# Kernel optimization log

Measured on AMD Instinct MI355X. Metric: run time of the kernel, lower is better.

The kernel has to match this reference:

```python
import jax, jax.numpy as jnp
from jax import lax
import numpy as np

GRID = 8
H384 = 6 * GRID * GRID  # 384, LSTM input and hidden size


def _conv(x, w, b):
    # x: [B,C,H,W], w: [O,I,kh,kw]
    y = lax.conv_general_dilated(x, w, (1, 1), 'VALID',
                                 dimension_numbers=('NCHW', 'OIHW', 'NCHW'))
    return y + b[None, :, None, None]


def _maxpool2(x):
    return lax.reduce_window(x, -jnp.inf, lax.max,
                             (1, 1, 2, 2), (1, 1, 2, 2), 'VALID')


def setup_inputs() -> dict:
    key = jax.random.key(0)
    ks = jax.random.split(key, 20)
    s = 0.05
    d = {
        'x': jax.random.normal(ks[0], (512, 100, 100), jnp.float32),
        # conv stack: Conv2d(1,16,7) ... Conv2d(128,128,3)
        'cw1': jax.random.normal(ks[1], (16, 1, 7, 7), jnp.float32) * s,
        'cb1': jnp.zeros((16,), jnp.float32),
        'cw2': jax.random.normal(ks[2], (32, 16, 4, 4), jnp.float32) * s,
        'cb2': jnp.zeros((32,), jnp.float32),
        'cw3': jax.random.normal(ks[3], (64, 32, 5, 5), jnp.float32) * s,
        'cb3': jnp.zeros((64,), jnp.float32),
        'cw4': jax.random.normal(ks[4], (128, 64, 5, 5), jnp.float32) * s,
        'cb4': jnp.zeros((128,), jnp.float32),
        'cw5': jax.random.normal(ks[5], (128, 128, 5, 5), jnp.float32) * s,
        'cb5': jnp.zeros((128,), jnp.float32),
        'cw6': jax.random.normal(ks[6], (128, 128, 3, 3), jnp.float32) * s,
        'cb6': jnp.zeros((128,), jnp.float32),
        # linear layers: 8192 -> 1024 -> 384, Sigmoid
        'lw1': jax.random.normal(ks[7], (1024, 8192), jnp.float32) * 0.01,
        'lb1': jnp.zeros((1024,), jnp.float32),
        'lw2': jax.random.normal(ks[8], (384, 1024), jnp.float32) * 0.02,
        'lb2': jnp.zeros((384,), jnp.float32),
        # LSTM (input 384, hidden 384, 1 layer), torch gate order i,f,g,o
        'w_ih': jax.random.normal(ks[9], (4 * H384, H384), jnp.float32) * s,
        'w_hh': jax.random.normal(ks[10], (4 * H384, H384), jnp.float32) * s,
        'b_ih': jnp.zeros((4 * H384,), jnp.float32),
        'b_hh': jnp.zeros((4 * H384,), jnp.float32),
    }
    return d


def reference(x, cw1, cb1, cw2, cb2, cw3, cb3, cw4, cb4, cw5, cb5, cw6, cb6,
              lw1, lb1, lw2, lb2, w_ih, w_hh, b_ih, b_hh):
    B = x.shape[0]
    h = x[:, None, :, :]                       # [B,1,100,100]
    h = _maxpool2(jax.nn.relu(_conv(h, cw1, cb1)))   # [B,16,47,47]
    h = _maxpool2(jax.nn.relu(_conv(h, cw2, cb2)))   # [B,32,22,22]
    h = jax.nn.relu(_conv(h, cw3, cb3))              # [B,64,18,18]
    h = jax.nn.relu(_conv(h, cw4, cb4))              # [B,128,14,14]
    h = jax.nn.relu(_conv(h, cw5, cb5))              # [B,128,10,10]
    h = jax.nn.relu(_conv(h, cw6, cb6))              # [B,128,8,8]
    h = h.reshape(B, -1)                             # [B,8192]
    h = h @ lw1.T + lb1                              # [B,1024]
    h = jax.nn.sigmoid(h @ lw2.T + lb2)              # [B,384]

    # Sequential LSTM over the batch dim with carried (h,c) state
    def step(carry, xt):
        hs, cs = carry
        gates = w_ih @ xt + b_ih + w_hh @ hs + b_hh  # [1536]
        i, f, g, o = jnp.split(gates, 4)
        cs = jax.nn.sigmoid(f) * cs + jax.nn.sigmoid(i) * jnp.tanh(g)
        hs = jax.nn.sigmoid(o) * jnp.tanh(cs)
        return (hs, cs), hs

    init = (jnp.zeros((H384,), x.dtype), jnp.zeros((H384,), x.dtype))
    _, ys = lax.scan(step, init, h)                  # [B,384]
    return ys.reshape(B, 6, GRID, GRID)
```

## Files before the change

kernel.cpp:

```cpp
#include <hip/hip_runtime.h>
#include <cstddef>
#include <cstdint>

#define T256 256

typedef __attribute__((ext_vector_type(8))) short bhalf8;
typedef __attribute__((ext_vector_type(4))) float floatx4;

__device__ __forceinline__ ushort f2bf(float f) {
  union { float f; uint32_t u; } v; v.f = f;
  return (ushort)((v.u + 0x7fffu + ((v.u >> 16) & 1u)) >> 16);
}

__device__ __forceinline__ float fsig(float x) {
  return 1.f / (1.f + __expf(-x));
}
__device__ __forceinline__ float ftanh(float x) {
  const float e = __expf(-2.f * fabsf(x));
  const float r = (1.f - e) / (1.f + e);
  return copysignf(r, x);
}

__global__ __launch_bounds__(256) void conv1_pool_k(
    const float* __restrict__ x, const float* __restrict__ w,
    const float* __restrict__ bias, float* __restrict__ out)
{
  __shared__ float img[10000];
  __shared__ float wsm[16 * 49];
  __shared__ float bsm[16];
  const int b = blockIdx.x, tid = threadIdx.x;
  for (int i = tid; i < 10000; i += T256) img[i] = x[(size_t)b * 10000 + i];
  for (int i = tid; i < 16 * 49; i += T256) wsm[i] = w[i];
  if (tid < 16) bsm[tid] = bias[tid];
  __syncthreads();
  for (int p = tid; p < 47 * 47; p += T256) {
    const int py = p / 47, px = p % 47;
    const int iy0 = 2 * py, ix0 = 2 * px;
    float win[8][8];
#pragma unroll
    for (int r = 0; r < 8; ++r)
#pragma unroll
      for (int c = 0; c < 8; ++c)
        win[r][c] = img[(iy0 + r) * 100 + (ix0 + c)];
#pragma unroll 1
    for (int oc = 0; oc < 16; ++oc) {
      float wr[49];
#pragma unroll
      for (int j = 0; j < 49; ++j) wr[j] = wsm[oc * 49 + j];
      float m = 0.f;
#pragma unroll
      for (int dy = 0; dy < 2; ++dy)
#pragma unroll
        for (int dx = 0; dx < 2; ++dx) {
          float s = bsm[oc];
#pragma unroll
          for (int ky = 0; ky < 7; ++ky)
#pragma unroll
            for (int kx = 0; kx < 7; ++kx)
              s += win[dy + ky][dx + kx] * wr[ky * 7 + kx];
          m = fmaxf(m, s);
        }
      out[((size_t)b * 16 + oc) * 2209 + p] = m;
    }
  }
}

__device__ __forceinline__ void wprep_one(
    const float* __restrict__ w, ushort* __restrict__ bswz,
    int IC, int KW, int OC, int idx)
{
  const int NT = OC / 16;
  const int lane = idx & 63;
  const int nt = (idx >> 6) % NT;
  const int ks = idx / (64 * NT);
  const int oc = nt * 16 + (lane & 15);
  const int kb = ks * 32 + (lane >> 4) * 8;
  ushort tmp[8];
#pragma unroll
  for (int j = 0; j < 8; ++j) {
    const int k = kb + j;
    const int ic = k % IC, tap = k / IC;
    tmp[j] = f2bf(w[((size_t)oc * IC + ic) * (KW * KW) + tap]);
  }
  *(bhalf8*)(bswz + (size_t)idx * 8) = *(const bhalf8*)tmp;
}

__global__ __launch_bounds__(256) void wprep_all_k(
    const float* __restrict__ cw2, const float* __restrict__ cw3,
    const float* __restrict__ cw4, const float* __restrict__ cw5,
    const float* __restrict__ cw6,
    ushort* __restrict__ bw2, ushort* __restrict__ bw3,
    ushort* __restrict__ bw4, ushort* __restrict__ bw5,
    ushort* __restrict__ bw6)
{
  int idx = blockIdx.x * 256 + threadIdx.x;
  if (idx < 6400)  { wprep_one(cw3, bw3, 32, 5, 64, idx); return; }
  idx -= 6400;
  if (idx < 25600) { wprep_one(cw4, bw4, 64, 5, 128, idx); return; }
  idx -= 25600;
  if (idx < 51200) { wprep_one(cw5, bw5, 128, 5, 128, idx); return; }
  idx -= 51200;
  if (idx < 18432) { wprep_one(cw6, bw6, 128, 3, 128, idx); return; }
  idx -= 18432;
  if (idx < 1024)  { wprep_one(cw2, bw2, 16, 4, 32, idx); }
}

__device__ __forceinline__ void wprep_lin_one(
    const float* __restrict__ w, ushort* __restrict__ bswz,
    int Kdim, int NT, int idx)
{
  const int lane = idx & 63;
  const int nt = (idx >> 6) % NT;
  const int ks = idx / (64 * NT);
  const int oc = nt * 16 + (lane & 15);
  const int kb = ks * 32 + (lane >> 4) * 8;
  ushort tmp[8];
#pragma unroll
  for (int j = 0; j < 8; ++j) tmp[j] = f2bf(w[(size_t)oc * Kdim + kb + j]);
  *(bhalf8*)(bswz + (size_t)idx * 8) = *(const bhalf8*)tmp;
}

__global__ __launch_bounds__(256) void wprep_lin3_k(
    const float* __restrict__ lw1, const float* __restrict__ lw2,
    const float* __restrict__ wih,
    ushort* __restrict__ bw1, ushort* __restrict__ bwl2,
    ushort* __restrict__ bwih)
{
  int idx = blockIdx.x * 256 + threadIdx.x;
  if (idx < 1048576) { wprep_lin_one(lw1, bw1, 8192, 64, idx); return; }
  idx -= 1048576;
  if (idx < 49152)   { wprep_lin_one(lw2, bwl2, 1024, 24, idx); return; }
  idx -= 49152;
  if (idx < 73728)   { wprep_lin_one(wih, bwih, 384, 96, idx); }
}

__global__ __launch_bounds__(256) void conv2mfma_k(
    const float* __restrict__ in, const ushort* __restrict__ bswz,
    const float* __restrict__ bias, float* __restrict__ out)
{
  constexpr int IC = 16, IH = 47, IW = 47;
  constexpr int NPIX = IH * IW;
  constexpr int ROWU = IC + 8;
  constexpr int KS = 8;
  __shared__ ushort imgT[NPIX * ROWU];
  const int b = blockIdx.x, tid = threadIdx.x;
  const int lane = tid & 63, wv = tid >> 6;

  for (int e = tid; e < IC * NPIX; e += 256) {
    const int ic = e / NPIX, pix = e % NPIX;
    imgT[pix * ROWU + ic] = f2bf(in[((size_t)b * IC + ic) * NPIX + pix]);
  }
  __syncthreads();

  const int col = lane & 15, g = lane >> 4;
  const float b0 = bias[col], b1 = bias[16 + col];

  for (int it = wv; it < 66; it += 4) {
    const int pyp = it / 3, tx = it - pyp * 3;
    int px = tx * 16 + col; px = px < 43 ? px : 43;
    floatx4 acc[2][2];
#pragma unroll
    for (int dy = 0; dy < 2; ++dy)
#pragma unroll
      for (int nt = 0; nt < 2; ++nt) acc[dy][nt] = (floatx4){0.f, 0.f, 0.f, 0.f};

    for (int ks = 0; ks < KS; ++ks) {
      bhalf8 bf[2];
#pragma unroll
      for (int nt = 0; nt < 2; ++nt)
        bf[nt] = *(const bhalf8*)(bswz + ((size_t)(ks * 2 + nt) * 64 + lane) * 8);
      const int kk = ks * 32 + g * 8;
      const int tap = kk >> 4, icb = kk & 15;
      const int ky = tap >> 2, kx = tap & 3;
      bhalf8 af[2];
#pragma unroll
      for (int dy = 0; dy < 2; ++dy)
        af[dy] = *(const bhalf8*)&imgT[((2 * pyp + dy + ky) * IW + px + kx) * ROWU + icb];
#pragma unroll
      for (int dy = 0; dy < 2; ++dy)
#pragma unroll
        for (int nt = 0; nt < 2; ++nt)
          acc[dy][nt] = __builtin_amdgcn_mfma_f32_16x16x32_bf16(
              af[dy], bf[nt], acc[dy][nt], 0, 0, 0);
    }
#pragma unroll
    for (int nt = 0; nt < 2; ++nt) {
      const int oc = nt * 16 + col;
      const float bb = nt ? b1 : b0;
      float vv[4];
#pragma unroll
      for (int i = 0; i < 4; ++i) vv[i] = fmaxf(acc[0][nt][i], acc[1][nt][i]);
#pragma unroll
      for (int q = 0; q < 2; ++q) {
        const int pxp = tx * 8 + g * 2 + q;
        if (pxp < 22) {
          const float v = fmaxf(fmaxf(vv[2 * q], vv[2 * q + 1]) + bb, 0.f);
          out[((size_t)b * 32 + oc) * 484 + pyp * 22 + pxp] = v;
        }
      }
    }
  }
}

template <int IC, int IH, int IW, int KW_, int OC, int MC>
__global__ __launch_bounds__(256) void convmfma_k(
    const float* __restrict__ in, const ushort* __restrict__ bswz,
    const float* __restrict__ bias, float* __restrict__ out)
{
  constexpr int OH = IH - KW_ + 1, OW = IW - KW_ + 1, P = OH * OW;
  constexpr int NPIX = IH * IW;
  constexpr int KS = IC * KW_ * KW_ / 32;
  constexpr int NT = OC / 16;
  constexpr int NPW = NT / 4;
  constexpr int MT = (P + 15) / 16;
  constexpr int ROWU = IC + 8;
  static_assert(NT % 4 == 0 && IC % 32 == 0, "cfg");

  __shared__ ushort imgT[NPIX * ROWU];
  const int b = blockIdx.x, tid = threadIdx.x;
  const int lane = tid & 63, wv = tid >> 6;
  const int icoff = (lane >> 4) * 8;

  for (int e = tid; e < IC * NPIX; e += 256) {
    const int ic = e / NPIX, pix = e % NPIX;
    imgT[pix * ROWU + ic] = f2bf(in[((size_t)b * IC + ic) * NPIX + pix]);
  }
  __syncthreads();

  for (int m0 = 0; m0 < MT; m0 += MC) {
    floatx4 acc[MC][NPW];
#pragma unroll
    for (int mi = 0; mi < MC; ++mi)
#pragma unroll
      for (int nn = 0; nn < NPW; ++nn)
        acc[mi][nn] = (floatx4){0.f, 0.f, 0.f, 0.f};

    int pbase[MC];
#pragma unroll
    for (int mi = 0; mi < MC; ++mi) {
      int p = (m0 + mi) * 16 + (lane & 15);
      p = p < P ? p : P - 1;
      pbase[mi] = ((p / OW) * IW + (p % OW)) * ROWU;
    }

    bhalf8 bcur[NPW];
#pragma unroll
    for (int nn = 0; nn < NPW; ++nn)
      bcur[nn] = *(const bhalf8*)(bswz + ((size_t)(wv * NPW + nn) * 64 + lane) * 8);

    for (int ks = 0; ks < KS; ++ks) {
      bhalf8 bnext[NPW];
      if (ks + 1 < KS) {
#pragma unroll
        for (int nn = 0; nn < NPW; ++nn)
          bnext[nn] = *(const bhalf8*)(bswz +
              ((size_t)((ks + 1) * NT + wv * NPW + nn) * 64 + lane) * 8);
      }
      const int tap = (ks * 32) / IC;
      const int icb = (ks * 32) % IC;
      const int aoff = ((tap / KW_) * IW + (tap % KW_)) * ROWU + icb + icoff;
      bhalf8 af[MC];
#pragma unroll
      for (int mi = 0; mi < MC; ++mi)
        af[mi] = *(const bhalf8*)&imgT[pbase[mi] + aoff];
#pragma unroll
      for (int mi = 0; mi < MC; ++mi)
#pragma unroll
        for (int nn = 0; nn < NPW; ++nn)
          acc[mi][nn] = __builtin_amdgcn_mfma_f32_16x16x32_bf16(
              af[mi], bcur[nn], acc[mi][nn], 0, 0, 0);
      if (ks + 1 < KS) {
#pragma unroll
        for (int nn = 0; nn < NPW; ++nn) bcur[nn] = bnext[nn];
      }
    }
#pragma unroll
    for (int mi = 0; mi < MC; ++mi)
#pragma unroll
      for (int nn = 0; nn < NPW; ++nn) {
        const int oc = (wv * NPW + nn) * 16 + (lane & 15);
#pragma unroll
        for (int i = 0; i < 4; ++i) {
          const int p = (m0 + mi) * 16 + (lane >> 4) * 4 + i;
          if (p < P) {
            const float v = fmaxf(acc[mi][nn][i] + bias[oc], 0.f);
            out[((size_t)b * OC + oc) * P + p] = v;
          }
        }
      }
  }
}

template <int ACT>
__global__ __launch_bounds__(256) void gemm_bf16_k(
    const float* __restrict__ A, const ushort* __restrict__ bswz,
    const float* __restrict__ b1, const float* __restrict__ b2,
    float* __restrict__ C, int M, int N, int K)
{
  __shared__ ushort As[64][72];
  const int bn = blockIdx.x, bm = blockIdx.y, tid = threadIdx.x;
  const int lane = tid & 63, wv = tid >> 6;
  const int m0 = bm * 64, n0 = bn * 64;
  const int NTg = N / 16;
  const int ntg = bn * 4 + wv;
  floatx4 acc[4];
#pragma unroll
  for (int mt = 0; mt < 4; ++mt) acc[mt] = (floatx4){0.f, 0.f, 0.f, 0.f};

  for (int kc = 0; kc < K / 64; ++kc) {
    __syncthreads();
#pragma unroll
    for (int q = 0; q < 2; ++q) {
      const int id = q * 256 + tid;
      const int row = id >> 3, kcol = (id & 7) * 8;
      const float* ap = &A[(size_t)(m0 + row) * K + kc * 64 + kcol];
      const float4 v0 = *(const float4*)ap;
      const float4 v1 = *(const float4*)(ap + 4);
      ushort t[8] = {f2bf(v0.x), f2bf(v0.y), f2bf(v0.z), f2bf(v0.w),
                     f2bf(v1.x), f2bf(v1.y), f2bf(v1.z), f2bf(v1.w)};
      *(bhalf8*)&As[row][kcol] = *(const bhalf8*)t;
    }
    __syncthreads();
#pragma unroll
    for (int k2 = 0; k2 < 2; ++k2) {
      const int ks = kc * 2 + k2;
      const bhalf8 bf = *(const bhalf8*)(bswz + ((size_t)(ks * NTg + ntg) * 64 + lane) * 8);
      const int ksub = k2 * 32 + (lane >> 4) * 8;
#pragma unroll
      for (int mt = 0; mt < 4; ++mt) {
        const bhalf8 af = *(const bhalf8*)&As[mt * 16 + (lane & 15)][ksub];
        acc[mt] = __builtin_amdgcn_mfma_f32_16x16x32_bf16(af, bf, acc[mt], 0, 0, 0);
      }
    }
  }
  const int n = n0 + wv * 16 + (lane & 15);
  const float bb = b1[n] + (b2 ? b2[n] : 0.f);
#pragma unroll
  for (int mt = 0; mt < 4; ++mt)
#pragma unroll
    for (int i = 0; i < 4; ++i) {
      const int m = m0 + mt * 16 + (lane >> 4) * 4 + i;
      float v = acc[mt][i] + bb;
      if (ACT == 1) v = 1.f / (1.f + expf(-v));
      C[(size_t)m * N + n] = v;
    }
}

#define NWG 16
#define CPW 24
__global__ __launch_bounds__(768) void lstm_k(
    const float* __restrict__ gin, const float* __restrict__ whh,
    float* __restrict__ out, unsigned long long* __restrict__ tagged)
{
  __shared__ __align__(16) float hsm[8][52];
  __shared__ float gsum[96];
  const int wg = blockIdx.x, tid = threadIdx.x;
  const int r = tid >> 3, lk = tid & 7;
  const int gq = r / CPW, cl = r % CPW;
  const int grow = gq * 384 + wg * CPW + cl;
  float wreg[48];
  {
    const float* wr = whh + (size_t)grow * 384 + lk * 48;
#pragma unroll
    for (int i = 0; i < 48; ++i) wreg[i] = wr[i];
  }
  float c = 0.f;
  if (tid < 64) __builtin_amdgcn_s_setprio(1);
  __syncthreads();
  for (int t = 0; t < 512; ++t) {
    float g0 = 0.f, g1 = 0.f, g2 = 0.f, g3 = 0.f;
    if (tid < CPW) {
      const int j = wg * CPW + tid;
      g0 = gin[(size_t)t * 1536 + 0 * 384 + j];
      g1 = gin[(size_t)t * 1536 + 1 * 384 + j];
      g2 = gin[(size_t)t * 1536 + 2 * 384 + j];
      g3 = gin[(size_t)t * 1536 + 3 * 384 + j];
    }
    if (tid < 384) {
      float hv;
      if (t == 0) {
        hv = 0.f;
      } else {
        unsigned long long u;
        do {
          u = __hip_atomic_load(&tagged[(size_t)(t - 1) * 384 + tid],
                                __ATOMIC_RELAXED, __HIP_MEMORY_SCOPE_AGENT);
        } while ((unsigned)(u >> 32) != (unsigned)t);
        union { unsigned ui; float f; } cv; cv.ui = (unsigned)u; hv = cv.f;
      }
      hsm[tid / 48][tid % 48] = hv;
    }
    __syncthreads();
    float s0 = 0.f, s1 = 0.f;
    {
      const float4* hp = (const float4*)&hsm[lk][0];
#pragma unroll
      for (int q = 0; q < 12; q += 2) {
        const float4 ha = hp[q], hb = hp[q + 1];
        s0 += wreg[4 * q + 0] * ha.x + wreg[4 * q + 1] * ha.y
            + wreg[4 * q + 2] * ha.z + wreg[4 * q + 3] * ha.w;
        s1 += wreg[4 * q + 4] * hb.x + wreg[4 * q + 5] * hb.y
            + wreg[4 * q + 6] * hb.z + wreg[4 * q + 7] * hb.w;
      }
    }
    float s = s0 + s1;
    s += __shfl_xor(s, 1);
    s += __shfl_xor(s, 2);
    s += __shfl_xor(s, 4);
    if (lk == 0) gsum[r] = s;
    __syncthreads();
    if (tid < CPW) {
      const float gi = gsum[0 * CPW + tid] + g0;
      const float gf = gsum[1 * CPW + tid] + g1;
      const float gg = gsum[2 * CPW + tid] + g2;
      const float go = gsum[3 * CPW + tid] + g3;
      const float si = fsig(gi);
      const float sf = fsig(gf);
      const float so = fsig(go);
      c = sf * c + si * ftanh(gg);
      const float hn = so * ftanh(c);
      const int j = wg * CPW + tid;
      union { float f; unsigned ui; } cv; cv.f = hn;
      const unsigned long long pk = ((unsigned long long)(t + 1) << 32) | cv.ui;
      __hip_atomic_store(&tagged[(size_t)t * 384 + j], pk,
                         __ATOMIC_RELAXED, __HIP_MEMORY_SCOPE_AGENT);
      out[(size_t)t * 384 + j] = hn;
    }
  }
}

extern "C" void kernel_launch(void* const* d_in, const int* in_sizes, int n_in,
                              void* d_out, int out_size, void* d_ws, size_t ws_size,
                              hipStream_t stream)
{
  const float* x   = (const float*)d_in[0];
  const float* cw1 = (const float*)d_in[1];
  const float* cb1 = (const float*)d_in[2];
  const float* cw2 = (const float*)d_in[3];
  const float* cb2 = (const float*)d_in[4];
  const float* cw3 = (const float*)d_in[5];
  const float* cb3 = (const float*)d_in[6];
  const float* cw4 = (const float*)d_in[7];
  const float* cb4 = (const float*)d_in[8];
  const float* cw5 = (const float*)d_in[9];
  const float* cb5 = (const float*)d_in[10];
  const float* cw6 = (const float*)d_in[11];
  const float* cb6 = (const float*)d_in[12];
  const float* lw1 = (const float*)d_in[13];
  const float* lb1 = (const float*)d_in[14];
  const float* lw2 = (const float*)d_in[15];
  const float* lb2 = (const float*)d_in[16];
  const float* wih = (const float*)d_in[17];
  const float* whh = (const float*)d_in[18];
  const float* bih = (const float*)d_in[19];
  const float* bhh = (const float*)d_in[20];
  float* out = (float*)d_out;
  char* ws = (char*)d_ws;

  float* bufA = (float*)(ws);
  float* bufB = (float*)(ws + 72384512);
  float* l1o  = (float*)(ws + 123764736);
  float* x2   = (float*)(ws + 125861888);
  float* gin  = (float*)(ws + 126648320);
  ushort* bw3 = (ushort*)(ws + 123764736);
  ushort* bw4 = (ushort*)(ws + 123764736 + 102400);
  ushort* bw5 = (ushort*)(ws + 123764736 + 512000);
  ushort* bw6 = (ushort*)(ws + 123764736 + 1331200);
  ushort* bw2 = (ushort*)(ws + 123764736 + 1626112);
  ushort* bw1  = (ushort*)(ws);
  unsigned long long* tagged = (unsigned long long*)(ws + 25165824);
  ushort* bwl2 = (ushort*)(ws + 26738688);
  ushort* bwih = (ushort*)(ws + 27525120);

  wprep_all_k<<<(102656 + 255) / 256, 256, 0, stream>>>(
      cw2, cw3, cw4, cw5, cw6, bw2, bw3, bw4, bw5, bw6);

  conv1_pool_k<<<512, 256, 0, stream>>>(x, cw1, cb1, bufA);
  conv2mfma_k<<<512, 256, 0, stream>>>(bufA, bw2, cb2, bufB);
  convmfma_k<32, 22, 22, 5, 64, 7><<<512, 256, 0, stream>>>(bufB, bw3, cb3, bufA);
  convmfma_k<64, 18, 18, 5, 128, 7><<<512, 256, 0, stream>>>(bufA, bw4, cb4, bufB);
  convmfma_k<128, 14, 14, 5, 128, 7><<<512, 256, 0, stream>>>(bufB, bw5, cb5, bufA);
  convmfma_k<128, 10, 10, 3, 128, 4><<<512, 256, 0, stream>>>(bufA, bw6, cb6, bufB);
  wprep_lin3_k<<<(1171456 + 255) / 256, 256, 0, stream>>>(
      lw1, lw2, wih, bw1, bwl2, bwih);
  hipMemsetAsync(tagged, 0, 512 * 384 * 8, stream);
  gemm_bf16_k<0><<<dim3(16, 8), 256, 0, stream>>>(bufB, bw1, lb1, nullptr, l1o, 512, 1024, 8192);
  gemm_bf16_k<1><<<dim3(6, 8), 256, 0, stream>>>(l1o, bwl2, lb2, nullptr, x2, 512, 384, 1024);
  gemm_bf16_k<0><<<dim3(24, 8), 256, 0, stream>>>(x2, bwih, bih, bhh, gin, 512, 1536, 384);
  lstm_k<<<NWG, 768, 0, stream>>>(gin, whh, out, tagged);
}
```

Baseline: 1.421 ms.

## Move conv1 with fused maxpool onto bf16 MFMA via even/odd shifted image copies

Replaces the scalar FP32 direct convolution for the first 7x7 conv layer with a bf16 MFMA formulation. The 7x7 kernel is zero-padded to 8x8 so K=64, split as two 16x16x32 MFMAs. The image is converted to bf16 in LDS as even- and odd-shifted copies so each lane can do aligned 4-byte loads. Conv weights are pre-swizzled in the existing weight-prep kernel, and the 2x2 maxpool, bias and ReLU are applied in registers after the MFMA. This is meant to remove the heavy per-thread FMA work of conv1, at the cost of bf16 rounding of the input image and extra LDS zeroing and fill work.

```diff
diff --git a/kernel.cpp b/kernel.cpp
--- a/kernel.cpp
+++ b/kernel.cpp
@@ -21,46 +21,64 @@
   return copysignf(r, x);
 }
 
-__global__ __launch_bounds__(256) void conv1_pool_k(
-    const float* __restrict__ x, const float* __restrict__ w,
+__global__ __launch_bounds__(256) void conv1mfma_k(
+    const float* __restrict__ x, const ushort* __restrict__ bswz,
     const float* __restrict__ bias, float* __restrict__ out)
 {
-  __shared__ float img[10000];
-  __shared__ float wsm[16 * 49];
-  __shared__ float bsm[16];
+  constexpr int W = 104;
+  constexpr int R = 101;
+  __shared__ __align__(16) ushort imgE[R * W];
+  __shared__ __align__(16) ushort imgO[R * W];
   const int b = blockIdx.x, tid = threadIdx.x;
-  for (int i = tid; i < 10000; i += T256) img[i] = x[(size_t)b * 10000 + i];
-  for (int i = tid; i < 16 * 49; i += T256) wsm[i] = w[i];
-  if (tid < 16) bsm[tid] = bias[tid];
+  const int lane = tid & 63, wv = tid >> 6;
+  const int col = lane & 15, g = lane >> 4;
+
+  for (int i = tid; i < R * W; i += 256) { imgE[i] = 0; imgO[i] = 0; }
   __syncthreads();
-  for (int p = tid; p < 47 * 47; p += T256) {
-    const int py = p / 47, px = p % 47;
-    const int iy0 = 2 * py, ix0 = 2 * px;
-    float win[8][8];
-#pragma unroll
-    for (int r = 0; r < 8; ++r)
-#pragma unroll
-      for (int c = 0; c < 8; ++c)
-        win[r][c] = img[(iy0 + r) * 100 + (ix0 + c)];
-#pragma unroll 1
-    for (int oc = 0; oc < 16; ++oc) {
-      float wr[49];
-#pragma unroll
-      for (int j = 0; j < 49; ++j) wr[j] = wsm[oc * 49 + j];
-      float m = 0.f;
-#pragma unroll
-      for (int dy = 0; dy < 2; ++dy)
-#pragma unroll
-        for (int dx = 0; dx < 2; ++dx) {
-          float s = bsm[oc];
-#pragma unroll
-          for (int ky = 0; ky < 7; ++ky)
-#pragma unroll
-            for (int kx = 0; kx < 7; ++kx)
-              s += win[dy + ky][dx + kx] * wr[ky * 7 + kx];
-          m = fmaxf(m, s);
-        }
-      out[((size_t)b * 16 + oc) * 2209 + p] = m;
+  for (int i = tid; i < 10000; i += 256) {
+    const int r = i / 100, c = i % 100;
+    const ushort v = f2bf(x[(size_t)b * 10000 + i]);
+    imgE[r * W + c] = v;
+    if (c >= 1) imgO[r * W + (c - 1)] = v;
+  }
+  __syncthreads();
+
+  const bhalf8 bf0 = *(const bhalf8*)(bswz + ((size_t)lane) * 8);
+  const bhalf8 bf1 = *(const bhalf8*)(bswz + ((size_t)(64 + lane)) * 8);
+  const float bb = bias[col];
+
+  for (int it = wv; it < 47 * 6; it += 4) {
+    const int pyp = it / 6, tx = it % 6;
+    int px = tx * 16 + col; px = px < 93 ? px : 93;
+    floatx4 acc[2];
+    acc[0] = (floatx4){0.f, 0.f, 0.f, 0.f};
+    acc[1] = (floatx4){0.f, 0.f, 0.f, 0.f};
+#pragma unroll
+    for (int ks = 0; ks < 2; ++ks) {
+      const int ky = ks * 4 + g;
+#pragma unroll
+      for (int dy = 0; dy < 2; ++dy) {
+        const int row = 2 * pyp + dy + ky;
+        const ushort* rowp = (px & 1) ? &imgO[row * W + px - 1] : &imgE[row * W + px];
+        union { uint32_t u[4]; bhalf8 v; } cvt;
+        cvt.u[0] = *(const uint32_t*)(rowp + 0);
+        cvt.u[1] = *(const uint32_t*)(rowp + 2);
+        cvt.u[2] = *(const uint32_t*)(rowp + 4);
+        cvt.u[3] = *(const uint32_t*)(rowp + 6);
+        acc[dy] = __builtin_amdgcn_mfma_f32_16x16x32_bf16(
+            cvt.v, ks ? bf1 : bf0, acc[dy], 0, 0, 0);
+      }
+    }
+    float vv[4];
+#pragma unroll
+    for (int i = 0; i < 4; ++i) vv[i] = fmaxf(acc[0][i], acc[1][i]);
+#pragma unroll
+    for (int q = 0; q < 2; ++q) {
+      const int pxp = tx * 8 + g * 2 + q;
+      if (pxp < 47) {
+        const float v = fmaxf(fmaxf(vv[2 * q], vv[2 * q + 1]) + bb, 0.f);
+        out[((size_t)b * 16 + col) * 2209 + pyp * 47 + pxp] = v;
+      }
     }
   }
 }
@@ -86,12 +104,12 @@
 }
 
 __global__ __launch_bounds__(256) void wprep_all_k(
-    const float* __restrict__ cw2, const float* __restrict__ cw3,
-    const float* __restrict__ cw4, const float* __restrict__ cw5,
-    const float* __restrict__ cw6,
-    ushort* __restrict__ bw2, ushort* __restrict__ bw3,
-    ushort* __restrict__ bw4, ushort* __restrict__ bw5,
-    ushort* __restrict__ bw6)
+    const float* __restrict__ cw1, const float* __restrict__ cw2,
+    const float* __restrict__ cw3, const float* __restrict__ cw4,
+    const float* __restrict__ cw5, const float* __restrict__ cw6,
+    ushort* __restrict__ bw1c, ushort* __restrict__ bw2,
+    ushort* __restrict__ bw3, ushort* __restrict__ bw4,
+    ushort* __restrict__ bw5, ushort* __restrict__ bw6)
 {
   int idx = blockIdx.x * 256 + threadIdx.x;
   if (idx < 6400)  { wprep_one(cw3, bw3, 32, 5, 64, idx); return; }
@@ -102,7 +120,22 @@
   idx -= 51200;
   if (idx < 18432) { wprep_one(cw6, bw6, 128, 3, 128, idx); return; }
   idx -= 18432;
-  if (idx < 1024)  { wprep_one(cw2, bw2, 16, 4, 32, idx); }
+  if (idx < 1024)  { wprep_one(cw2, bw2, 16, 4, 32, idx); return; }
+  idx -= 1024;
+  if (idx < 128) {
+    const int lane = idx & 63;
+    const int ks = idx >> 6;
+    const int oc = lane & 15;
+    const int kb = ks * 32 + (lane >> 4) * 8;
+    ushort tmp[8];
+#pragma unroll
+    for (int j = 0; j < 8; ++j) {
+      const int k = kb + j;
+      const int ky = k >> 3, kx = k & 7;
+      tmp[j] = (ky < 7 && kx < 7) ? f2bf(cw1[oc * 49 + ky * 7 + kx]) : (ushort)0;
+    }
+    *(bhalf8*)(bw1c + (size_t)idx * 8) = *(const bhalf8*)tmp;
+  }
 }
 
 __device__ __forceinline__ void wprep_lin_one(
@@ -467,15 +500,16 @@
   ushort* bw5 = (ushort*)(ws + 123764736 + 512000);
   ushort* bw6 = (ushort*)(ws + 123764736 + 1331200);
   ushort* bw2 = (ushort*)(ws + 123764736 + 1626112);
+  ushort* bw1c = (ushort*)(ws + 123764736 + 1642496);
   ushort* bw1  = (ushort*)(ws);
   unsigned long long* tagged = (unsigned long long*)(ws + 25165824);
   ushort* bwl2 = (ushort*)(ws + 26738688);
   ushort* bwih = (ushort*)(ws + 27525120);
 
-  wprep_all_k<<<(102656 + 255) / 256, 256, 0, stream>>>(
-      cw2, cw3, cw4, cw5, cw6, bw2, bw3, bw4, bw5, bw6);
-
-  conv1_pool_k<<<512, 256, 0, stream>>>(x, cw1, cb1, bufA);
+  wprep_all_k<<<(102784 + 255) / 256, 256, 0, stream>>>(
+      cw1, cw2, cw3, cw4, cw5, cw6, bw1c, bw2, bw3, bw4, bw5, bw6);
+
+  conv1mfma_k<<<512, 256, 0, stream>>>(x, bw1c, cb1, bufA);
   conv2mfma_k<<<512, 256, 0, stream>>>(bufA, bw2, cb2, bufB);
   convmfma_k<32, 22, 22, 5, 64, 7><<<512, 256, 0, stream>>>(bufB, bw3, cb3, bufA);
   convmfma_k<64, 18, 18, 5, 128, 7><<<512, 256, 0, stream>>>(bufA, bw4, cb4, bufB);
```

After: 1.346 ms. -5.3%, faster.
